# Optimization experiments

Measured on AMD Instinct MI355X. Metric: run time of the kernel, lower is better.

## Reference

```python
import jax, jax.numpy as jnp
import numpy as np

N_IN, N_OUT, GRID_SIZE = 2048, 2048, 8

def setup_inputs() -> dict:
    key = jax.random.key(0)
    k1, k2 = jax.random.split(key)
    x = jax.random.normal(k1, (4096, N_IN), dtype=jnp.float32)
    coef = 0.1 * jax.random.normal(k2, (N_IN, N_OUT, GRID_SIZE), dtype=jnp.float32)
    grid = jnp.linspace(-1.0, 1.0, GRID_SIZE).astype(jnp.float32)
    return {"x": x, "coef": coef, "grid": grid}

def reference(x, coef, grid):
    # basis: [B, n_in, grid_size] gaussian bumps around grid points
    basis = jnp.exp(-5.0 * (x[..., None] - grid[None, None, :]) ** 2)
    basis = basis / (jnp.sum(basis, axis=-1, keepdims=True) + 1e-8)
    # y_j = sum_i sum_k basis[b,i,k] * coef[i,j,k]
    out = jnp.einsum('bik,ijk->bj', basis, coef)
    return out
```

## Files before the change

kernel.cpp:

```cpp
#include <hip/hip_runtime.h>
#include <hip/hip_bf16.h>

#define BATCH   4096
#define NIN     2048
#define NOUT    2048
#define GS      8

typedef __attribute__((ext_vector_type(8))) short  bf16x8;
typedef __attribute__((ext_vector_type(4))) short  bf16x4;
typedef __attribute__((ext_vector_type(4))) float  f32x4;

__device__ __forceinline__ short f2bf(float f) {
    unsigned u = __builtin_bit_cast(unsigned, f);
    u += 0x7fffu + ((u >> 16) & 1u);
    return (short)(u >> 16);
}

__device__ __forceinline__ bf16x8 basis_bf16(float xv, const float* g) {
    const float KE = -7.2134752044448170f;
    float e[GS], s = 0.f;
#pragma unroll
    for (int k = 0; k < GS; ++k) {
        float t = xv - g[k];
        e[k] = __builtin_amdgcn_exp2f(t * t * KE);
        s += e[k];
    }
    float rn = __builtin_amdgcn_rcpf(s + 1e-8f);
    bf16x8 fr;
#pragma unroll
    for (int k = 0; k < GS; ++k) fr[k] = f2bf(e[k] * rn);
    return fr;
}

__device__ __forceinline__ void async16(const void* g, void* l) {
    __builtin_amdgcn_global_load_lds(
        (const __attribute__((address_space(1))) unsigned*)g,
        (__attribute__((address_space(3))) unsigned*)l, 16, 0, 0);
}

#define PREP_BLOCKS 4096
#define TB 64
#define TI 32

__global__ __launch_bounds__(256, 4)
void kan_prep_kernel(const float* __restrict__ x, const float* __restrict__ coef,
                     const float* __restrict__ grid,
                     short* __restrict__ A_ws, short* __restrict__ B_ws)
{
    const int t = threadIdx.x;

    for (int c = blockIdx.x; c < (NIN * NOUT * GS) / 4096; c += PREP_BLOCKS) {
        const float* src = coef + (size_t)c * 4096;
        short*       dst = B_ws + (size_t)c * 4096;
        f32x4 v[4];
#pragma unroll
        for (int j = 0; j < 4; ++j)
            v[j] = __builtin_nontemporal_load((const f32x4*)(src + j * 1024 + t * 4));
#pragma unroll
        for (int j = 0; j < 4; ++j) {
            bf16x4 o;
#pragma unroll
            for (int k = 0; k < 4; ++k) o[k] = f2bf(v[j][k]);
            *(bf16x4*)(dst + j * 1024 + t * 4) = o;
        }
    }

    __shared__ float tile[TB][TI + 1];
    float g[GS];
#pragma unroll
    for (int k = 0; k < GS; ++k) g[k] = grid[k];

    for (int job = blockIdx.x; job < (NIN / TI) * (BATCH / TB); job += PREP_BLOCKS) {
        const int i0 = (job & (NIN / TI - 1)) * TI;
        const int b0 = (job / (NIN / TI)) * TB;
        __syncthreads();
#pragma unroll
        for (int p = 0; p < (TB * TI) / 256; ++p) {
            int idx = t + p * 256;
            int b_l = idx >> 5, i_l = idx & 31;
            tile[b_l][i_l] = x[(size_t)(b0 + b_l) * NIN + i0 + i_l];
        }
        __syncthreads();
#pragma unroll
        for (int it = 0; it < 8; ++it) {
            int b_l = (t & 31) + 32 * (it & 1);
            int i_l = (t >> 5) + 8 * (it >> 1);
            bf16x8 fr = basis_bf16(tile[b_l][i_l], g);
            *(bf16x8*)(A_ws + (size_t)(i0 + i_l) * (BATCH * GS)
                            + (size_t)(b0 + b_l) * GS) = fr;
        }
    }
}

__global__ __launch_bounds__(256, 4)
void kan_gemm_splitk(const short* __restrict__ A_ws, const short* __restrict__ B_ws,
                     float* __restrict__ P)
{
    __shared__ __align__(16) char As[16384];
    __shared__ __align__(16) char Bs[16384];

    const int t    = threadIdx.x;
    const int wave = t >> 6;
    const int lane = t & 63;
    const int l15  = lane & 15;
    const int quad = lane >> 4;
    const int wm = wave & 1, wn = wave >> 1;
    const int m_blk = blockIdx.x * 128, n_blk = blockIdx.y * 128;
    const int z = blockIdx.z;

    f32x4 acc[4][4];
#pragma unroll
    for (int a = 0; a < 4; ++a)
#pragma unroll
        for (int b = 0; b < 4; ++b)
            acc[a][b] = (f32x4){0.f, 0.f, 0.f, 0.f};

    const char* Abase = (const char*)A_ws + (size_t)m_blk * (GS * 2);
    const char* Bbase = (const char*)B_ws + (size_t)n_blk * (GS * 2);
    const size_t strideA = (size_t)BATCH * GS * 2;
    const size_t strideB = (size_t)NOUT  * GS * 2;

    int dma_off[4], dma_iloc[4], dma_rem[4];
#pragma unroll
    for (int j = 0; j < 4; ++j) {
        dma_off[j]  = j * 4096 + t * 16;
        dma_iloc[j] = dma_off[j] >> 11;
        dma_rem[j]  = dma_off[j] & 2047;
    }

    const int i_lo = z * (NIN / 2), i_hi = i_lo + (NIN / 2);
    for (int i0 = i_lo; i0 < i_hi; i0 += 8) {
#pragma unroll
        for (int j = 0; j < 4; ++j) {
            const size_t i = (size_t)(i0 + dma_iloc[j]);
            async16(Abase + i * strideA + dma_rem[j], As + dma_off[j]);
            async16(Bbase + i * strideB + dma_rem[j], Bs + dma_off[j]);
        }
        __syncthreads();

#pragma unroll
        for (int s = 0; s < 2; ++s) {
            const int iloc = s * 4 + quad;
            bf16x8 af[4], bf[4];
#pragma unroll
            for (int ms = 0; ms < 4; ++ms)
                af[ms] = *(const bf16x8*)(As + (size_t)(iloc * 128 + wm * 64 + ms * 16 + l15) * 16);
#pragma unroll
            for (int ns = 0; ns < 4; ++ns)
                bf[ns] = *(const bf16x8*)(Bs + (size_t)(iloc * 128 + wn * 64 + ns * 16 + l15) * 16);
#pragma unroll
            for (int ms = 0; ms < 4; ++ms)
#pragma unroll
                for (int ns = 0; ns < 4; ++ns)
                    acc[ms][ns] = __builtin_amdgcn_mfma_f32_16x16x32_bf16(
                        af[ms], bf[ns], acc[ms][ns], 0, 0, 0);
        }
        __syncthreads();
    }

    float* Pz = P + (size_t)z * ((size_t)BATCH * NOUT);
    const int m_base = m_blk + wm * 64;
    const int n_base = n_blk + wn * 64;
#pragma unroll
    for (int ms = 0; ms < 4; ++ms)
#pragma unroll
        for (int ns = 0; ns < 4; ++ns) {
            const int col = n_base + ns * 16 + l15;
#pragma unroll
            for (int r = 0; r < 4; ++r) {
                const int row = m_base + ms * 16 + quad * 4 + r;
                Pz[(size_t)row * NOUT + col] = acc[ms][ns][r];
            }
        }
}

__global__ __launch_bounds__(256, 4)
void kan_reduce_kernel(const float* __restrict__ P, float* __restrict__ out)
{
    const size_t n4 = (size_t)BATCH * NOUT / 4;
    for (size_t idx = (size_t)blockIdx.x * 256 + threadIdx.x; idx < n4;
         idx += (size_t)1024 * 256) {
        f32x4 a = ((const f32x4*)P)[idx];
        f32x4 b = ((const f32x4*)P)[idx + n4];
        ((f32x4*)out)[idx] = a + b;
    }
}

__global__ __launch_bounds__(256, 2)
void kan_gemm_kernel(const short* __restrict__ A_ws, const short* __restrict__ B_ws,
                     float* __restrict__ out)
{
    __shared__ __align__(16) char As[16384];
    __shared__ __align__(16) char Bs[16384];

    const int t    = threadIdx.x;
    const int wave = t >> 6;
    const int lane = t & 63;
    const int l15  = lane & 15;
    const int quad = lane >> 4;
    const int wm = wave & 1, wn = wave >> 1;
    const int m_blk = blockIdx.x * 128, n_blk = blockIdx.y * 128;

    f32x4 acc[4][4];
#pragma unroll
    for (int a = 0; a < 4; ++a)
#pragma unroll
        for (int b = 0; b < 4; ++b)
            acc[a][b] = (f32x4){0.f, 0.f, 0.f, 0.f};

    const char* Abase = (const char*)A_ws + (size_t)m_blk * (GS * 2);
    const char* Bbase = (const char*)B_ws + (size_t)n_blk * (GS * 2);
    const size_t strideA = (size_t)BATCH * GS * 2;
    const size_t strideB = (size_t)NOUT  * GS * 2;

    int dma_off[4], dma_iloc[4], dma_rem[4];
#pragma unroll
    for (int j = 0; j < 4; ++j) {
        dma_off[j]  = j * 4096 + t * 16;
        dma_iloc[j] = dma_off[j] >> 11;
        dma_rem[j]  = dma_off[j] & 2047;
    }

    for (int i0 = 0; i0 < NIN; i0 += 8) {
#pragma unroll
        for (int j = 0; j < 4; ++j) {
            const size_t i = (size_t)(i0 + dma_iloc[j]);
            async16(Abase + i * strideA + dma_rem[j], As + dma_off[j]);
            async16(Bbase + i * strideB + dma_rem[j], Bs + dma_off[j]);
        }
        __syncthreads();
#pragma unroll
        for (int s = 0; s < 2; ++s) {
            const int iloc = s * 4 + quad;
            bf16x8 af[4], bf[4];
#pragma unroll
            for (int ms = 0; ms < 4; ++ms)
                af[ms] = *(const bf16x8*)(As + (size_t)(iloc * 128 + wm * 64 + ms * 16 + l15) * 16);
#pragma unroll
            for (int ns = 0; ns < 4; ++ns)
                bf[ns] = *(const bf16x8*)(Bs + (size_t)(iloc * 128 + wn * 64 + ns * 16 + l15) * 16);
#pragma unroll
            for (int ms = 0; ms < 4; ++ms)
#pragma unroll
                for (int ns = 0; ns < 4; ++ns)
                    acc[ms][ns] = __builtin_amdgcn_mfma_f32_16x16x32_bf16(
                        af[ms], bf[ns], acc[ms][ns], 0, 0, 0);
        }
        __syncthreads();
    }

    const int m_base = m_blk + wm * 64;
    const int n_base = n_blk + wn * 64;
#pragma unroll
    for (int ms = 0; ms < 4; ++ms)
#pragma unroll
        for (int ns = 0; ns < 4; ++ns) {
            const int col = n_base + ns * 16 + l15;
#pragma unroll
            for (int r = 0; r < 4; ++r) {
                const int row = m_base + ms * 16 + quad * 4 + r;
                out[(size_t)row * NOUT + col] = acc[ms][ns][r];
            }
        }
}

__global__ __launch_bounds__(256, 2)
void kan_fused_kernel(const float* __restrict__ x, const float* __restrict__ coef,
                      const float* __restrict__ grid, float* __restrict__ out)
{
    const int tid  = threadIdx.x;
    const int wave = tid >> 6;
    const int lane = tid & 63;
    const int l15  = lane & 15;
    const int quad = lane >> 4;
    const int m_base = blockIdx.x * 128 + (wave & 1) * 64;
    const int n_base = blockIdx.y * 128 + (wave >> 1) * 64;

    float g[GS];
#pragma unroll
    for (int k = 0; k < GS; ++k) g[k] = grid[k];

    f32x4 acc[4][4];
#pragma unroll
    for (int a = 0; a < 4; ++a)
#pragma unroll
        for (int b = 0; b < 4; ++b) acc[a][b] = (f32x4){0.f, 0.f, 0.f, 0.f};

    const float* xp = x + (size_t)(m_base + l15) * NIN + quad;
    const float* cp = coef + (size_t)quad * (NOUT * GS) + (size_t)(n_base + l15) * GS;

    for (int i0 = 0; i0 < NIN; i0 += 4) {
        f32x4 braw[4][2];
#pragma unroll
        for (int ns = 0; ns < 4; ++ns) {
            const float* p = cp + ns * (16 * GS);
            braw[ns][0] = *(const f32x4*)(p);
            braw[ns][1] = *(const f32x4*)(p + 4);
        }
        bf16x8 afrag[4];
#pragma unroll
        for (int ms = 0; ms < 4; ++ms)
            afrag[ms] = basis_bf16(xp[ms * 16 * NIN], g);
        bf16x8 bfrag[4];
#pragma unroll
        for (int ns = 0; ns < 4; ++ns) {
            bf16x8 fr;
#pragma unroll
            for (int k = 0; k < 4; ++k) { fr[k] = f2bf(braw[ns][0][k]); fr[k+4] = f2bf(braw[ns][1][k]); }
            bfrag[ns] = fr;
        }
#pragma unroll
        for (int ms = 0; ms < 4; ++ms)
#pragma unroll
            for (int ns = 0; ns < 4; ++ns)
                acc[ms][ns] = __builtin_amdgcn_mfma_f32_16x16x32_bf16(
                    afrag[ms], bfrag[ns], acc[ms][ns], 0, 0, 0);
        xp += 4;
        cp += 4 * (NOUT * GS);
    }
#pragma unroll
    for (int ms = 0; ms < 4; ++ms)
#pragma unroll
        for (int ns = 0; ns < 4; ++ns) {
            const int col = n_base + ns * 16 + l15;
#pragma unroll
            for (int r = 0; r < 4; ++r)
                out[(size_t)(m_base + ms * 16 + quad * 4 + r) * NOUT + col] = acc[ms][ns][r];
        }
}

extern "C" void kernel_launch(void* const* d_in, const int* in_sizes, int n_in,
                              void* d_out, int out_size, void* d_ws, size_t ws_size,
                              hipStream_t stream) {
    const float* x    = (const float*)d_in[0];
    const float* coef = (const float*)d_in[1];
    const float* grid = (const float*)d_in[2];
    float* out        = (float*)d_out;

    const size_t a_elems = (size_t)NIN * BATCH * GS;
    const size_t b_elems = (size_t)NIN * NOUT * GS;
    const size_t p_elems = (size_t)2 * BATCH * NOUT;
    const size_t need_basic  = (a_elems + b_elems) * sizeof(short);
    const size_t need_splitk = need_basic + p_elems * sizeof(float);

    if (ws_size >= need_basic) {
        short* A_ws = (short*)d_ws;
        short* B_ws = A_ws + a_elems;

        kan_prep_kernel<<<PREP_BLOCKS, 256, 0, stream>>>(x, coef, grid, A_ws, B_ws);

        if (ws_size >= need_splitk) {
            float* P = (float*)(B_ws + b_elems);
            dim3 g2(BATCH / 128, NOUT / 128, 2);
            kan_gemm_splitk<<<g2, 256, 0, stream>>>(A_ws, B_ws, P);
            kan_reduce_kernel<<<1024, 256, 0, stream>>>(P, out);
        } else {
            dim3 g2(BATCH / 128, NOUT / 128);
            kan_gemm_kernel<<<g2, 256, 0, stream>>>(A_ws, B_ws, out);
        }
    } else {
        dim3 grd(BATCH / 128, NOUT / 128);
        kan_fused_kernel<<<grd, 256, 0, stream>>>(x, coef, grid, out);
    }
}
```

Measured before the change: 498.8 us.

## Store split-K partials in bf16 and split prep blocks between coef and basis

The split-K GEMM now writes its partial sums as bf16 instead of fp32, and the reduce kernel reads eight bf16 values per thread and widens them to fp32 before adding. This halves the partial-buffer write and read traffic. The prep kernel also changes: half its blocks convert coef to bf16 while the other half compute the basis tiles, so each block does only one kind of work rather than both in sequence. The cost is lower accuracy, since partial sums are rounded to bf16 before the final add.

```diff
diff --git a/kernel.cpp b/kernel.cpp
--- a/kernel.cpp
+++ b/kernel.cpp
@@ -15,6 +15,10 @@
     u += 0x7fffu + ((u >> 16) & 1u);
     return (short)(u >> 16);
 }
+__device__ __forceinline__ float bf2f(short s) {
+    unsigned u = ((unsigned)(unsigned short)s) << 16;
+    return __builtin_bit_cast(float, u);
+}
 
 __device__ __forceinline__ bf16x8 basis_bf16(float xv, const float* g) {
     const float KE = -7.2134752044448170f;
@@ -47,30 +51,34 @@
                      const float* __restrict__ grid,
                      short* __restrict__ A_ws, short* __restrict__ B_ws)
 {
+    __shared__ float tile[TB][TI + 1];
     const int t = threadIdx.x;
 
-    for (int c = blockIdx.x; c < (NIN * NOUT * GS) / 4096; c += PREP_BLOCKS) {
-        const float* src = coef + (size_t)c * 4096;
-        short*       dst = B_ws + (size_t)c * 4096;
-        f32x4 v[4];
-#pragma unroll
-        for (int j = 0; j < 4; ++j)
-            v[j] = __builtin_nontemporal_load((const f32x4*)(src + j * 1024 + t * 4));
-#pragma unroll
-        for (int j = 0; j < 4; ++j) {
-            bf16x4 o;
-#pragma unroll
-            for (int k = 0; k < 4; ++k) o[k] = f2bf(v[j][k]);
-            *(bf16x4*)(dst + j * 1024 + t * 4) = o;
-        }
-    }
-
-    __shared__ float tile[TB][TI + 1];
+    if (blockIdx.x < PREP_BLOCKS / 2) {
+        for (int c = blockIdx.x; c < (NIN * NOUT * GS) / 4096; c += PREP_BLOCKS / 2) {
+            const float* src = coef + (size_t)c * 4096;
+            short*       dst = B_ws + (size_t)c * 4096;
+            f32x4 v[4];
+#pragma unroll
+            for (int j = 0; j < 4; ++j)
+                v[j] = __builtin_nontemporal_load((const f32x4*)(src + j * 1024 + t * 4));
+#pragma unroll
+            for (int j = 0; j < 4; ++j) {
+                bf16x4 o;
+#pragma unroll
+                for (int k = 0; k < 4; ++k) o[k] = f2bf(v[j][k]);
+                *(bf16x4*)(dst + j * 1024 + t * 4) = o;
+            }
+        }
+        return;
+    }
+
     float g[GS];
 #pragma unroll
     for (int k = 0; k < GS; ++k) g[k] = grid[k];
 
-    for (int job = blockIdx.x; job < (NIN / TI) * (BATCH / TB); job += PREP_BLOCKS) {
+    for (int job = blockIdx.x - PREP_BLOCKS / 2; job < (NIN / TI) * (BATCH / TB);
+         job += PREP_BLOCKS / 2) {
         const int i0 = (job & (NIN / TI - 1)) * TI;
         const int b0 = (job / (NIN / TI)) * TB;
         __syncthreads();
@@ -94,7 +102,7 @@
 
 __global__ __launch_bounds__(256, 4)
 void kan_gemm_splitk(const short* __restrict__ A_ws, const short* __restrict__ B_ws,
-                     float* __restrict__ P)
+                     short* __restrict__ P)
 {
     __shared__ __align__(16) char As[16384];
     __shared__ __align__(16) char Bs[16384];
@@ -158,7 +166,7 @@
         __syncthreads();
     }
 
-    float* Pz = P + (size_t)z * ((size_t)BATCH * NOUT);
+    short* Pz = P + (size_t)z * ((size_t)BATCH * NOUT);
     const int m_base = m_blk + wm * 64;
     const int n_base = n_blk + wn * 64;
 #pragma unroll
@@ -169,20 +177,27 @@
 #pragma unroll
             for (int r = 0; r < 4; ++r) {
                 const int row = m_base + ms * 16 + quad * 4 + r;
-                Pz[(size_t)row * NOUT + col] = acc[ms][ns][r];
+                Pz[(size_t)row * NOUT + col] = f2bf(acc[ms][ns][r]);
             }
         }
 }
 
 __global__ __launch_bounds__(256, 4)
-void kan_reduce_kernel(const float* __restrict__ P, float* __restrict__ out)
-{
-    const size_t n4 = (size_t)BATCH * NOUT / 4;
-    for (size_t idx = (size_t)blockIdx.x * 256 + threadIdx.x; idx < n4;
+void kan_reduce_kernel(const short* __restrict__ P, float* __restrict__ out)
+{
+    const size_t n8 = (size_t)BATCH * NOUT / 8;
+    for (size_t idx = (size_t)blockIdx.x * 256 + threadIdx.x; idx < n8;
          idx += (size_t)1024 * 256) {
-        f32x4 a = ((const f32x4*)P)[idx];
-        f32x4 b = ((const f32x4*)P)[idx + n4];
-        ((f32x4*)out)[idx] = a + b;
+        bf16x8 a = ((const bf16x8*)P)[idx];
+        bf16x8 b = ((const bf16x8*)P)[idx + n8];
+        f32x4 o0, o1;
+#pragma unroll
+        for (int k = 0; k < 4; ++k) {
+            o0[k] = bf2f(a[k])     + bf2f(b[k]);
+            o1[k] = bf2f(a[k + 4]) + bf2f(b[k + 4]);
+        }
+        ((f32x4*)out)[idx * 2]     = o0;
+        ((f32x4*)out)[idx * 2 + 1] = o1;
     }
 }
 
@@ -341,7 +356,7 @@
     const size_t b_elems = (size_t)NIN * NOUT * GS;
     const size_t p_elems = (size_t)2 * BATCH * NOUT;
     const size_t need_basic  = (a_elems + b_elems) * sizeof(short);
-    const size_t need_splitk = need_basic + p_elems * sizeof(float);
+    const size_t need_splitk = need_basic + p_elems * sizeof(short);
 
     if (ws_size >= need_basic) {
         short* A_ws = (short*)d_ws;
@@ -350,7 +365,7 @@
         kan_prep_kernel<<<PREP_BLOCKS, 256, 0, stream>>>(x, coef, grid, A_ws, B_ws);
 
         if (ws_size >= need_splitk) {
-            float* P = (float*)(B_ws + b_elems);
+            short* P = B_ws + b_elems;
             dim3 g2(BATCH / 128, NOUT / 128, 2);
             kan_gemm_splitk<<<g2, 256, 0, stream>>>(A_ws, B_ws, P);
             kan_reduce_kernel<<<1024, 256, 0, stream>>>(P, out);
```

After: 489.8 us. Within noise of the previous version (-1.8%).
